# Kernel tuning notes

Hardware: AMD Instinct MI355X
Metric: run time of the kernel (lower is better)

Reference implementation:

```python
import jax, jax.numpy as jnp
import numpy as np

# Hard-coded dims from MambaLayer.__init__
D_IN = 20        # input feature dim (Dense infers it; chosen = modelInternalDim)
D_INNER = 20     # modelInternalDim
N_STATES = 10    # modelStates
DT_RANK = 5      # delta_t_rank
BATCH = 4
SEQ = 32768


def setup_inputs() -> dict:
    key = jax.random.key(0)
    ks = jax.random.split(key, 8)
    s = lambda k, shape: jax.random.normal(k, shape, dtype=jnp.float32) * 0.05
    A = jnp.tile(jnp.arange(1, N_STATES + 1, dtype=jnp.float32)[None, :], (D_INNER, 1))
    return {
        "x": jax.random.normal(ks[0], (BATCH, SEQ, D_IN), dtype=jnp.float32),
        "w_in": s(ks[1], (D_IN, 2 * D_INNER)),
        "b_in": jnp.zeros((2 * D_INNER,), jnp.float32),
        "conv_k": s(ks[2], (3, D_INNER, D_INNER)),   # (W, I, O)
        "conv_b": jnp.zeros((D_INNER,), jnp.float32),
        "w_x": s(ks[3], (D_INNER, DT_RANK + 2 * N_STATES)),
        "b_x": jnp.zeros((DT_RANK + 2 * N_STATES,), jnp.float32),
        "w_dt": s(ks[4], (DT_RANK, D_INNER)),
        "b_dt": jnp.zeros((D_INNER,), jnp.float32),
        "A_log": jnp.log(A),
        "D_param": jnp.ones((D_INNER,), jnp.float32),
    }


def _selective_scan(u, delta, A, B, C, D):
    # u, delta: (b,l,d); A: (d,n); B, C: (b,l,n); D: (d,)
    dA = jnp.einsum('bld,dn->bldn', delta, A)                  # (b,l,d,n)
    dB_u = jnp.einsum('bld,bld,bln->bldn', delta, u, B)        # (b,l,d,n)
    # tf.pad(dA[:,1:], [[0,0],[1,1],...])[:,1:] == concat(dA[:,1:], zeros) along l
    dA_shift = jnp.concatenate([dA[:, 1:], jnp.zeros_like(dA[:, :1])], axis=1)
    # reversed cumsum, exponentiate, reverse back
    dA_cumsum = jnp.exp(jnp.flip(jnp.cumsum(jnp.flip(dA_shift, axis=1), axis=1), axis=1))
    x = jnp.cumsum(dB_u * dA_cumsum, axis=1) / (dA_cumsum + 1e-12)
    y = jnp.einsum('bldn,bln->bld', x, C)
    return y + u * D


def reference(x, w_in, b_in, conv_k, conv_b, w_x, b_x, w_dt, b_dt, A_log, D_param):
    # in_projection + split (res half is unused, matching the original call())
    h = x @ w_in + b_in                                        # (b,l,2d)
    h, _res = jnp.split(h, 2, axis=-1)
    # causal Conv1D, kernel_size=3: left-pad by 2
    h = jax.lax.conv_general_dilated(
        h, conv_k, window_strides=(1,), padding=[(2, 0)],
        dimension_numbers=('NWC', 'WIO', 'NWC')) + conv_b
    h = jax.nn.silu(h)                                         # tf.nn.swish
    # ssm
    A = -jnp.exp(A_log)                                        # (d,n)
    xp = h @ w_x + b_x                                         # (b,l,r+2n)
    delta = xp[..., :DT_RANK]
    Bm = xp[..., DT_RANK:DT_RANK + N_STATES]
    Cm = xp[..., DT_RANK + N_STATES:]
    delta = jax.nn.softmax(delta @ w_dt + b_dt, axis=-1)       # (b,l,d)
    return _selective_scan(h, delta, A, Bm, Cm, D_param)
```

## Files before the change

kernel.cpp:

```cpp
#include <hip/hip_runtime.h>
#include <math.h>

#define B_   4
#define L_   32768
#define DI   20
#define NS   10
#define TBLK 128
#define NCB  256

#define OFF_AP   0u
#define OFF_RS   204800u
#define OFF_SC   409600u
#define OFF_TOT  430080u
#define OFF_H16  430192u
#define OFF_CMIN 4362352u
#define HD  0u
#define HU  2621440u
#define HB  5242880u
#define HC  6553600u

typedef _Float16 h16;
typedef _Float16 half8 __attribute__((ext_vector_type(8)));
typedef _Float16 half4 __attribute__((ext_vector_type(4)));
typedef float f32x4 __attribute__((ext_vector_type(4)));

template<int CTRL>
__device__ __forceinline__ float dppf(float idv, float src) {
    union U { float f; int i; };
    U o, s, r; o.f = idv; s.f = src;
    r.i = __builtin_amdgcn_update_dpp(o.i, s.i, CTRL, 0xf, 0xf, false);
    return r.f;
}
#define ROW_SHR1 0x111
#define ROW_SHR2 0x112
#define ROW_SHR4 0x114
#define ROW_SHR8 0x118

#define OPSCAN16(Ac, Bc) \
    { float aP = dppf<ROW_SHR1>(1.0f, Ac); float bP = dppf<ROW_SHR1>(0.0f, Bc); \
      Bc = fmaf(Ac, bP, Bc); Ac *= aP; \
      aP = dppf<ROW_SHR2>(1.0f, Ac); bP = dppf<ROW_SHR2>(0.0f, Bc); \
      Bc = fmaf(Ac, bP, Bc); Ac *= aP; \
      aP = dppf<ROW_SHR4>(1.0f, Ac); bP = dppf<ROW_SHR4>(0.0f, Bc); \
      Bc = fmaf(Ac, bP, Bc); Ac *= aP; \
      aP = dppf<ROW_SHR8>(1.0f, Ac); bP = dppf<ROW_SHR8>(0.0f, Bc); \
      Bc = fmaf(Ac, bP, Bc); Ac *= aP; }

#define SUMSCAN16(v) \
    { v += dppf<ROW_SHR1>(0.0f, v); v += dppf<ROW_SHR2>(0.0f, v); \
      v += dppf<ROW_SHR4>(0.0f, v); v += dppf<ROW_SHR8>(0.0f, v); }

#define XS_   0
#define MT_   2640
#define UL_   0
#define DS__  0
#define DUS_  2720
#define XP5_  4608
#define BS_   5448
#define WXo   6808
#define WDTo  7808
#define BDTo  7908
#define BXo   7928
#define POOLH 7956
#define WF_   7956
#define POOL2 (POOLH + 3200)

__global__ __launch_bounds__(320) void k1(
    const float* __restrict__ x,
    const float* __restrict__ w_in, const float* __restrict__ b_in,
    const float* __restrict__ conv_k, const float* __restrict__ conv_b,
    const float* __restrict__ w_x, const float* __restrict__ b_x,
    const float* __restrict__ w_dt, const float* __restrict__ b_dt,
    const float* __restrict__ A_log, const float* __restrict__ D_param,
    h16* __restrict__ dh, h16* __restrict__ uh,
    h16* __restrict__ Bh, h16* __restrict__ Ch,
    float* __restrict__ ap_ws, float* __restrict__ rs_ws, float* __restrict__ sc_ws,
    float* __restrict__ out)
{
    __shared__ __align__(16) h16 P[POOL2];
    __shared__ float beff_s[20];
    __shared__ float ALs[200];
    __shared__ float D_s[20];

    const int tid = threadIdx.x;
    const int c   = blockIdx.x;
    const int b   = blockIdx.y;
    const int l0  = c * TBLK;

    {
        float* Wf = (float*)&P[WF_];
        for (int i = tid; i < 400;  i += 320) Wf[i]       = w_in[(i/20)*40 + (i%20)];
        for (int i = tid; i < 1200; i += 320) Wf[400 + i] = conv_k[i];
        for (int i = tid; i < 200;  i += 320) ALs[i] = -__expf(A_log[i]);
        if (tid < 20) D_s[tid] = D_param[tid];
    }
    __syncthreads();

    {
        const float* Wf = (const float*)&P[WF_];
        for (int e = tid; e < 1200; e += 320) {
            int cc = e/20, o = e - cc*20;
            int w = cc/20, i = cc - w*20;
            float acc = 0.0f;
            #pragma unroll
            for (int op = 0; op < 20; op++)
                acc = fmaf(Wf[i*20 + op], Wf[400 + (w*20 + op)*20 + o], acc);
            P[MT_ + o*72 + cc] = (h16)acc;
        }
        for (int i = tid; i < 240; i += 320) {
            int o = i/12, cc = 60 + (i - (i/12)*12);
            P[MT_ + o*72 + cc] = (h16)0.0f;
        }
        for (int i = tid; i < 1000; i += 320) {
            int j = i/40, k = i - j*40;
            P[WXo + i] = (k < 20) ? (h16)w_x[k*25 + j] : (h16)0.0f;
        }
        for (int i = tid; i < 100; i += 320) P[WDTo + i] = (h16)w_dt[i];
        if (tid < 20) P[BDTo + tid] = (h16)b_dt[tid];
        if (tid < 25) P[BXo + tid] = (h16)b_x[tid];
        if (tid < 20) {
            float be = conv_b[tid];
            #pragma unroll
            for (int w = 0; w < 3; w++)
                #pragma unroll
                for (int op = 0; op < 20; op++)
                    be = fmaf(b_in[op], Wf[400 + (w*20 + op)*20 + tid], be);
            beff_s[tid] = be;
        }
        const float* xb = x + ((size_t)b*L_ + l0)*DI - 2*DI;
        for (int i = tid; i < 1320; i += 320) {
            float2 v;
            if (i >= 1300 || (c == 0 && i < 20)) v = make_float2(0.0f, 0.0f);
            else v = *(const float2*)(xb + 2*i);
            P[XS_ + 2*i]     = (h16)v.x;
            P[XS_ + 2*i + 1] = (h16)v.y;
        }
    }
    __syncthreads();

    const int wv  = tid >> 6;
    const int ln  = tid & 63;
    const int m16 = ln & 15;
    const int q   = ln >> 4;
    float uval[4][4];
    if (wv < 4) {
        #pragma unroll
        for (int jj = 0; jj < 4; jj++) {
            int job = wv*4 + jj, mt = job >> 1, nt = job & 1;
            int t_row = mt*16 + m16;
            int dcol  = nt*16 + m16;
            int dmin  = dcol < 20 ? dcol : 19;
            f32x4 acc = {0.0f, 0.0f, 0.0f, 0.0f};
            #pragma unroll
            for (int kh = 0; kh < 2; kh++) {
                half8 af, bf;
                int ab = XS_ + t_row*20 + kh*32 + (q<<3);
                *(half4*)&af         = *(const half4*)&P[ab];
                *(((half4*)&af) + 1) = *(const half4*)&P[ab + 4];
                int bb = MT_ + dmin*72 + kh*32 + (q<<3);
                *(half4*)&bf         = *(const half4*)&P[bb];
                *(((half4*)&bf) + 1) = *(const half4*)&P[bb + 4];
                acc = __builtin_amdgcn_mfma_f32_16x16x32_f16(af, bf, acc, 0, 0, 0);
            }
            float bfv = beff_s[dmin];
            #pragma unroll
            for (int r = 0; r < 4; r++) {
                float a = acc[r] + bfv;
                uval[jj][r] = a * __builtin_amdgcn_rcpf(1.0f + __expf(-a));
            }
        }
    }
    __syncthreads();

    if (wv < 4) {
        #pragma unroll
        for (int jj = 0; jj < 4; jj++) {
            int job = wv*4 + jj, mt = job >> 1, nt = job & 1;
            int dcol = nt*16 + m16;
            if (dcol < 20) {
                #pragma unroll
                for (int r = 0; r < 4; r++)
                    P[UL_ + (mt*16 + q*4 + r)*36 + dcol] = (h16)uval[jj][r];
            }
        }
    }
    __syncthreads();

    float xv[4][4];
    if (wv < 4) {
        #pragma unroll
        for (int jj = 0; jj < 4; jj++) {
            int job = wv*4 + jj, mt = job >> 1, nt = job & 1;
            int t_row = mt*16 + m16;
            int j     = nt*16 + m16;
            int jmin  = j < 25 ? j : 24;
            f32x4 acc = {0.0f, 0.0f, 0.0f, 0.0f};
            half8 af, bf;
            int ab = UL_ + t_row*36 + (q<<3);
            *(half4*)&af         = *(const half4*)&P[ab];
            *(((half4*)&af) + 1) = *(const half4*)&P[ab + 4];
            int bb = WXo + jmin*40 + (q<<3);
            *(half4*)&bf         = *(const half4*)&P[bb];
            *(((half4*)&bf) + 1) = *(const half4*)&P[bb + 4];
            acc = __builtin_amdgcn_mfma_f32_16x16x32_f16(af, bf, acc, 0, 0, 0);
            float bx = (j < 25) ? (float)P[BXo + j] : 0.0f;
            #pragma unroll
            for (int r = 0; r < 4; r++) xv[jj][r] = acc[r] + bx;
        }
        #pragma unroll
        for (int jj = 0; jj < 4; jj++) {
            int job = wv*4 + jj, mt = job >> 1, nt = job & 1;
            int j = nt*16 + m16;
            #pragma unroll
            for (int r = 0; r < 4; r++) {
                int t = mt*16 + q*4 + r;
                h16 hv = (h16)xv[jj][r];
                if (j < 5)       P[XP5_ + t*5 + j] = hv;
                else if (j < 15) P[BS_ + (j - 5)*136 + t] = hv;
                else if (j < 25) Ch[(size_t)(b*NS + (j - 15))*L_ + l0 + t] = hv;
            }
        }
    }
    __syncthreads();

    h16 urow[20];
    float dl[20];
    if (tid < 128) {
        const int t = tid;
        *(half4*)&urow[0]  = *(const half4*)&P[UL_ + t*36 + 0];
        *(half4*)&urow[4]  = *(const half4*)&P[UL_ + t*36 + 4];
        *(half4*)&urow[8]  = *(const half4*)&P[UL_ + t*36 + 8];
        *(half4*)&urow[12] = *(const half4*)&P[UL_ + t*36 + 12];
        *(half4*)&urow[16] = *(const half4*)&P[UL_ + t*36 + 16];
        #pragma unroll
        for (int d2 = 0; d2 < 20; d2++)
            uh[(size_t)(b*DI + d2)*L_ + l0 + t] = urow[d2];
        #pragma unroll
        for (int n = 0; n < NS; n++)
            Bh[(size_t)(b*NS + n)*L_ + l0 + t] = P[BS_ + n*136 + t];
        {
            float yo[20];
            #pragma unroll
            for (int d2 = 0; d2 < 20; d2++) yo[d2] = (float)urow[d2] * D_s[d2];
            float4* ob = (float4*)(out + ((size_t)b*L_ + l0 + t)*DI);
            #pragma unroll
            for (int k4 = 0; k4 < 5; k4++)
                ob[k4] = make_float4(yo[4*k4], yo[4*k4+1], yo[4*k4+2], yo[4*k4+3]);
        }
        float xq[5];
        #pragma unroll
        for (int r = 0; r < 5; r++) xq[r] = (float)P[XP5_ + t*5 + r];
        #pragma unroll
        for (int d2 = 0; d2 < 20; d2++) dl[d2] = (float)P[BDTo + d2];
        #pragma unroll
        for (int r = 0; r < 5; r++) {
            float dv = xq[r];
            #pragma unroll
            for (int d2 = 0; d2 < 20; d2++)
                dl[d2] = fmaf(dv, (float)P[WDTo + r*20 + d2], dl[d2]);
        }
        float mx = dl[0];
        #pragma unroll
        for (int d2 = 1; d2 < 20; d2++) mx = fmaxf(mx, dl[d2]);
        float sm = 0.0f;
        #pragma unroll
        for (int d2 = 0; d2 < 20; d2++) { dl[d2] = __expf(dl[d2] - mx); sm += dl[d2]; }
        float inv = __builtin_amdgcn_rcpf(sm);
        #pragma unroll
        for (int d2 = 0; d2 < 20; d2++) dl[d2] *= inv;
    }
    __syncthreads();

    if (tid < 128) {
        const int t = tid;
        #pragma unroll
        for (int d2 = 0; d2 < 20; d2++) {
            h16 dlh = (h16)dl[d2];
            P[DS__ + d2*136 + t] = dlh;
            P[DUS_ + d2*136 + t] = (h16)((float)dlh * (float)urow[d2]);
            dh[(size_t)(b*DI + d2)*L_ + l0 + t] = dlh;
        }
    }
    __syncthreads();

    const int d  = tid >> 4;
    const int s  = tid & 15;
    const int bd = b*DI + d;

    float d8[8], du8[8];
    { half8 hv = *(const half8*)&P[DS__ + d*136 + 8*s];
      #pragma unroll
      for (int j = 0; j < 8; j++) d8[j] = (float)hv[j]; }
    { half8 hv = *(const half8*)&P[DUS_ + d*136 + 8*s];
      #pragma unroll
      for (int j = 0; j < 8; j++) du8[j] = (float)hv[j]; }

    float loc8 = 0.0f;
    #pragma unroll
    for (int j = 0; j < 8; j++) loc8 += d8[j];
    float ssum = loc8;
    SUMSCAN16(ssum);
    if (s == 15) sc_ws[(size_t)bd*NCB + c] = ssum;

    float A_dn[NS];
    #pragma unroll
    for (int n = 0; n < NS; n++) A_dn[n] = ALs[d*NS + n];

    bool fastA = true;
    #pragma unroll
    for (int n = 1; n < NS; n++)
        fastA = fastA &&
            (fabsf(A_dn[n] - (float)(n+1)*A_dn[0]) <= 1e-3f*fabsf(A_dn[n]) + 1e-6f);

    float AcA[NS], BcA[NS];
    if (fastA) {
        float e1[8], ep[8];
        #pragma unroll
        for (int j = 0; j < 8; j++) { e1[j] = __expf(A_dn[0]*d8[j]); ep[j] = e1[j]; }
        #pragma unroll
        for (int n = 0; n < NS; n++) {
            half8 bv = *(const half8*)&P[BS_ + n*136 + 8*s];
            float Bc = 0.0f;
            #pragma unroll
            for (int j = 0; j < 8; j++)
                Bc = fmaf(ep[j], Bc, du8[j]*(float)bv[j]);
            BcA[n] = Bc;
            AcA[n] = __expf(A_dn[n]*loc8);
            if (n < NS-1) {
                #pragma unroll
                for (int j = 0; j < 8; j++) ep[j] *= e1[j];
            }
        }
    } else {
        #pragma unroll
        for (int n = 0; n < NS; n++) {
            half8 bv = *(const half8*)&P[BS_ + n*136 + 8*s];
            float Bc = 0.0f;
            #pragma unroll
            for (int j = 0; j < 8; j++) {
                float a = __expf(A_dn[n]*d8[j]);
                Bc = fmaf(a, Bc, du8[j]*(float)bv[j]);
            }
            BcA[n] = Bc;
            AcA[n] = __expf(A_dn[n]*loc8);
        }
    }
    #pragma unroll
    for (int n = 0; n < NS; n++) { OPSCAN16(AcA[n], BcA[n]); }
    if (s == 15) {
        const size_t o0 = ((size_t)bd*NS)*NCB + c;
        #pragma unroll
        for (int n = 0; n < NS; n++) {
            ap_ws[o0 + (size_t)n*NCB] = AcA[n];
            rs_ws[o0 + (size_t)n*NCB] = BcA[n];
        }
    }
}

__global__ __launch_bounds__(64) void kC2(
    const float* __restrict__ ap_ws, float* __restrict__ rs_ws,
    float* __restrict__ sc_ws, float* __restrict__ tot_ws,
    const float* __restrict__ A_log, float* __restrict__ cmin_ws)
{
    const int bd   = blockIdx.x;
    const int lane = threadIdx.x;
    const size_t sb = (size_t)bd*NCB + lane*4;

    float4 sv = *(const float4*)(sc_ws + sb);
    float l1 = sv.x, l2 = l1 + sv.y, l3 = l2 + sv.z, l4 = l3 + sv.w;
    float inc = l4;
    #pragma unroll
    for (int off = 1; off < 64; off <<= 1) {
        float t = __shfl_up(inc, off);
        if (lane >= off) inc += t;
    }
    float ex = __shfl_up(inc, 1);
    if (lane == 0) ex = 0.0f;
    *(float4*)(sc_ws + sb) = make_float4(ex, ex + l1, ex + l2, ex + l3);
    if (lane == 63) tot_ws[bd] = inc;

    {
        const float TotAll = __shfl(inc, 63);
        const int dd = bd % DI;
        float mnlog = A_log[dd*NS];
        #pragma unroll
        for (int n = 1; n < NS; n++) mnlog = fminf(mnlog, A_log[dd*NS + n]);
        const float Amax = -__expf(mnlog);
        int cand = 100000;
        if (fmaf(Amax, TotAll - (ex + l4), 40.0f) > 0.0f) cand = lane*4 + 3;
        if (fmaf(Amax, TotAll - (ex + l3), 40.0f) > 0.0f) cand = lane*4 + 2;
        if (fmaf(Amax, TotAll - (ex + l2), 40.0f) > 0.0f) cand = lane*4 + 1;
        if (fmaf(Amax, TotAll - (ex + l1), 40.0f) > 0.0f) cand = lane*4 + 0;
        #pragma unroll
        for (int off = 32; off > 0; off >>= 1)
            cand = min(cand, __shfl_xor(cand, off));
        if (lane == 0) cmin_ws[bd] = (float)cand;
    }

    #pragma unroll 2
    for (int n = 0; n < NS; n++) {
        const size_t base = ((size_t)bd*NS + n)*NCB + lane*4;
        float4 av = *(const float4*)(ap_ws + base);
        float4 rv = *(const float4*)(rs_ws + base);
        float Ac = av.x, Bc = rv.x;
        Bc = fmaf(av.y, Bc, rv.y); Ac *= av.y;
        Bc = fmaf(av.z, Bc, rv.z); Ac *= av.z;
        Bc = fmaf(av.w, Bc, rv.w); Ac *= av.w;
        #pragma unroll
        for (int off = 1; off < 64; off <<= 1) {
            float aP = __shfl_up(Ac, off);
            float bP = __shfl_up(Bc, off);
            if (lane >= off) { Bc = fmaf(Ac, bP, Bc); Ac *= aP; }
        }
        float pB = __shfl_up(Bc, 1);
        if (lane == 0) pB = 0.0f;
        float r  = pB;
        float o0 = r; r = fmaf(av.x, r, rv.x);
        float o1 = r; r = fmaf(av.y, r, rv.y);
        float o2 = r; r = fmaf(av.z, r, rv.z);
        float o3 = r;
        *(float4*)(rs_ws + base) = make_float4(o0, o1, o2, o3);
    }
}

__global__ __launch_bounds__(320) void kD(
    const h16* __restrict__ dh, const h16* __restrict__ uh,
    const h16* __restrict__ Bh, const h16* __restrict__ Ch,
    const float* __restrict__ A_log, const float* __restrict__ D_param,
    const float* __restrict__ rs_ws, const float* __restrict__ sc_ws,
    const float* __restrict__ tot_ws, const float* __restrict__ cmin_ws,
    float* __restrict__ out)
{
    __shared__ float ylT[20*132];
    __shared__ int anyact;
    const int tid = threadIdx.x;
    const int d   = tid >> 4;
    const int s   = tid & 15;
    const int c   = blockIdx.x;
    const int b   = blockIdx.y;
    const int bd  = b*DI + d;
    const size_t t0 = (size_t)c*TBLK + s*8;

    const bool active = (c >= (int)cmin_ws[bd]);

    if (tid == 0) anyact = 0;
    __syncthreads();
    if (active) anyact = 1;
    __syncthreads();
    if (anyact == 0) return;

    float u8[8];
    { half8 hv = *(const half8*)(uh + (size_t)bd*L_ + t0);
      #pragma unroll
      for (int j = 0; j < 8; j++) u8[j] = (float)hv[j]; }
    const float Dd = D_param[d];
    float yv[8];
    #pragma unroll
    for (int j = 0; j < 8; j++) yv[j] = u8[j]*Dd;

    if (active) {
        half8 dvv = *(const half8*)(dh + (size_t)bd*L_ + t0);
        half8 bvA[NS], cvA[NS];
        #pragma unroll
        for (int n = 0; n < NS; n++) {
            bvA[n] = *(const half8*)(Bh + (size_t)(b*NS + n)*L_ + t0);
            cvA[n] = *(const half8*)(Ch + (size_t)(b*NS + n)*L_ + t0);
        }
        float rin[NS];
        #pragma unroll
        for (int n = 0; n < NS; n++) rin[n] = rs_ws[((size_t)bd*NS + n)*NCB + c];
        const float Tot = tot_ws[bd];
        const float scc = sc_ws[(size_t)bd*NCB + c];
        float A_dn[NS];
        #pragma unroll
        for (int n = 0; n < NS; n++) A_dn[n] = -__expf(A_log[d*NS + n]);

        bool fastA = true;
        #pragma unroll
        for (int n = 1; n < NS; n++)
            fastA = fastA &&
                (fabsf(A_dn[n] - (float)(n+1)*A_dn[0]) <= 1e-3f*fabsf(A_dn[n]) + 1e-6f);

        float d8[8], du8[8];
        #pragma unroll
        for (int j = 0; j < 8; j++) { d8[j] = (float)dvv[j]; du8[j] = d8[j]*u8[j]; }

        float lp[8];
        { float run = 0.0f;
          #pragma unroll
          for (int j = 0; j < 8; j++) { run += d8[j]; lp[j] = run; } }
        float inc = lp[7];
        SUMSCAN16(inc);
        float ex = dppf<ROW_SHR1>(0.0f, inc);
        const float basep = scc + ex;

        float yacc[8];
        #pragma unroll
        for (int j = 0; j < 8; j++) yacc[j] = 0.0f;

        if (fastA) {
            float e1[8], ep[8];
            #pragma unroll
            for (int j = 0; j < 8; j++) { e1[j] = __expf(A_dn[0]*d8[j]); ep[j] = e1[j]; }
            #pragma unroll
            for (int n = 0; n < NS; n++) {
                float b8[8];
                #pragma unroll
                for (int j = 0; j < 8; j++) b8[j] = du8[j]*(float)bvA[n][j];
                float Bc = 0.0f;
                #pragma unroll
                for (int j = 0; j < 8; j++) Bc = fmaf(ep[j], Bc, b8[j]);
                float Ac = __expf(A_dn[n]*lp[7]);
                OPSCAN16(Ac, Bc);
                float pA = dppf<ROW_SHR1>(1.0f, Ac);
                float pB = dppf<ROW_SHR1>(0.0f, Bc);
                float r  = fmaf(pA, rin[n], pB);

                float G[8];
                G[7] = __expf(A_dn[n]*(Tot - (basep + lp[7])));
                #pragma unroll
                for (int j = 6; j >= 0; j--) G[j] = G[j+1]*ep[j+1];
                #pragma unroll
                for (int j = 0; j < 8; j++) {
                    r = fmaf(ep[j], r, b8[j]);
                    float damp = G[j] * __builtin_amdgcn_rcpf(G[j] + 1e-12f);
                    yacc[j] = fmaf((float)cvA[n][j]*damp, r, yacc[j]);
                }
                if (n < NS-1) {
                    #pragma unroll
                    for (int j = 0; j < 8; j++) ep[j] *= e1[j];
                }
            }
        } else {
            #pragma unroll 2
            for (int n = 0; n < NS; n++) {
                float a8[8], b8[8];
                #pragma unroll
                for (int j = 0; j < 8; j++) {
                    a8[j] = __expf(A_dn[n]*d8[j]);
                    b8[j] = du8[j]*(float)bvA[n][j];
                }
                float Bc = 0.0f;
                #pragma unroll
                for (int j = 0; j < 8; j++) Bc = fmaf(a8[j], Bc, b8[j]);
                float Ac = __expf(A_dn[n]*lp[7]);
                OPSCAN16(Ac, Bc);
                float pA = dppf<ROW_SHR1>(1.0f, Ac);
                float pB = dppf<ROW_SHR1>(0.0f, Bc);
                float r  = fmaf(pA, rin[n], pB);

                float G[8];
                G[7] = __expf(A_dn[n]*(Tot - (basep + lp[7])));
                #pragma unroll
                for (int j = 6; j >= 0; j--) G[j] = G[j+1]*a8[j+1];
                #pragma unroll
                for (int j = 0; j < 8; j++) {
                    r = fmaf(a8[j], r, b8[j]);
                    float damp = G[j] * __builtin_amdgcn_rcpf(G[j] + 1e-12f);
                    yacc[j] = fmaf((float)cvA[n][j]*damp, r, yacc[j]);
                }
            }
        }
        #pragma unroll
        for (int j = 0; j < 8; j++) yv[j] = fmaf(u8[j], Dd, yacc[j]);
    }

    *(float4*)&ylT[d*132 + 8*s]     = *(float4*)(yv);
    *(float4*)&ylT[d*132 + 8*s + 4] = *(float4*)(yv + 4);
    __syncthreads();

    float4* ob4 = (float4*)(out + ((size_t)b*L_ + (size_t)c*TBLK)*DI);
    for (int i = tid; i < TBLK*DI/4; i += 320) {
        int t = i / 5, qq = (i - t*5)*4;
        ob4[i] = make_float4(ylT[qq*132 + t], ylT[(qq+1)*132 + t],
                             ylT[(qq+2)*132 + t], ylT[(qq+3)*132 + t]);
    }
}

extern "C" void kernel_launch(void* const* d_in, const int* in_sizes, int n_in,
                              void* d_out, int out_size, void* d_ws, size_t ws_size,
                              hipStream_t stream) {
    const float* x      = (const float*)d_in[0];
    const float* w_in   = (const float*)d_in[1];
    const float* b_in   = (const float*)d_in[2];
    const float* conv_k = (const float*)d_in[3];
    const float* conv_b = (const float*)d_in[4];
    const float* w_x    = (const float*)d_in[5];
    const float* b_x    = (const float*)d_in[6];
    const float* w_dt   = (const float*)d_in[7];
    const float* b_dt   = (const float*)d_in[8];
    const float* A_log  = (const float*)d_in[9];
    const float* D_par  = (const float*)d_in[10];
    float* out = (float*)d_out;
    float* ws  = (float*)d_ws;

    float* ap_ws   = ws + OFF_AP;
    float* rs_ws   = ws + OFF_RS;
    float* sc_ws   = ws + OFF_SC;
    float* tot_ws  = ws + OFF_TOT;
    float* cmin_ws = ws + OFF_CMIN;
    h16*   hbase   = (h16*)(ws + OFF_H16);
    h16* dh  = hbase + HD;
    h16* uh  = hbase + HU;
    h16* Bh  = hbase + HB;
    h16* Ch  = hbase + HC;

    k1<<<dim3(NCB, B_), 320, 0, stream>>>(x, w_in, b_in, conv_k, conv_b,
                                          w_x, b_x, w_dt, b_dt, A_log, D_par,
                                          dh, uh, Bh, Ch,
                                          ap_ws, rs_ws, sc_ws, out);
    kC2<<<B_*DI, 64, 0, stream>>>(ap_ws, rs_ws, sc_ws, tot_ws, A_log, cmin_ws);
    kD<<<dim3(NCB, B_), 320, 0, stream>>>(dh, uh, Bh, Ch, A_log, D_par,
                                          rs_ws, sc_ws, tot_ws, cmin_ws, out);
}
```

Before: 123.6 us.

## Fuse carry scan and tail output pass into one per-channel kernel

Merges the chunk-carry scan kernel and the output kernel into a single kernel with one 64-thread block per (batch, channel). Scanned prefix sums and carries stay in shared memory instead of going back to the workspace. Each block then loops only over its own active tail chunks, four at a time, and writes outputs directly. This removes one launch and several workspace round trips, and drops the grid of mostly-idle output blocks. The cost is far less parallelism for the tail work, since only 80 small blocks run, and output stores are now strided per channel instead of coalesced through a shared-memory transpose.

```diff
diff --git a/kernel.cpp b/kernel.cpp
--- a/kernel.cpp
+++ b/kernel.cpp
@@ -11,9 +11,7 @@
 #define OFF_AP   0u
 #define OFF_RS   204800u
 #define OFF_SC   409600u
-#define OFF_TOT  430080u
 #define OFF_H16  430192u
-#define OFF_CMIN 4362352u
 #define HD  0u
 #define HU  2621440u
 #define HB  5242880u
@@ -357,15 +355,22 @@
     }
 }
 
-__global__ __launch_bounds__(64) void kC2(
-    const float* __restrict__ ap_ws, float* __restrict__ rs_ws,
-    float* __restrict__ sc_ws, float* __restrict__ tot_ws,
-    const float* __restrict__ A_log, float* __restrict__ cmin_ws)
+__global__ __launch_bounds__(64) void kC3(
+    const float* __restrict__ ap_ws, const float* __restrict__ rs_ws,
+    const float* __restrict__ sc_ws, const float* __restrict__ A_log,
+    const float* __restrict__ D_param,
+    const h16* __restrict__ dh, const h16* __restrict__ uh,
+    const h16* __restrict__ Bh, const h16* __restrict__ Ch,
+    float* __restrict__ out)
 {
+    __shared__ float sc_l[NCB];
+    __shared__ float rs_l[NS][NCB];
     const int bd   = blockIdx.x;
     const int lane = threadIdx.x;
+    const int b    = bd / DI;
+    const int d    = bd - b*DI;
+
     const size_t sb = (size_t)bd*NCB + lane*4;
-
     float4 sv = *(const float4*)(sc_ws + sb);
     float l1 = sv.x, l2 = l1 + sv.y, l3 = l2 + sv.z, l4 = l3 + sv.w;
     float inc = l4;
@@ -376,26 +381,21 @@
     }
     float ex = __shfl_up(inc, 1);
     if (lane == 0) ex = 0.0f;
-    *(float4*)(sc_ws + sb) = make_float4(ex, ex + l1, ex + l2, ex + l3);
-    if (lane == 63) tot_ws[bd] = inc;
-
-    {
-        const float TotAll = __shfl(inc, 63);
-        const int dd = bd % DI;
-        float mnlog = A_log[dd*NS];
-        #pragma unroll
-        for (int n = 1; n < NS; n++) mnlog = fminf(mnlog, A_log[dd*NS + n]);
-        const float Amax = -__expf(mnlog);
-        int cand = 100000;
-        if (fmaf(Amax, TotAll - (ex + l4), 40.0f) > 0.0f) cand = lane*4 + 3;
-        if (fmaf(Amax, TotAll - (ex + l3), 40.0f) > 0.0f) cand = lane*4 + 2;
-        if (fmaf(Amax, TotAll - (ex + l2), 40.0f) > 0.0f) cand = lane*4 + 1;
-        if (fmaf(Amax, TotAll - (ex + l1), 40.0f) > 0.0f) cand = lane*4 + 0;
-        #pragma unroll
-        for (int off = 32; off > 0; off >>= 1)
-            cand = min(cand, __shfl_xor(cand, off));
-        if (lane == 0) cmin_ws[bd] = (float)cand;
-    }
+    *(float4*)(&sc_l[lane*4]) = make_float4(ex, ex + l1, ex + l2, ex + l3);
+    const float Tot = __shfl(inc, 63);
+
+    float mnlog = A_log[d*NS];
+    #pragma unroll
+    for (int n = 1; n < NS; n++) mnlog = fminf(mnlog, A_log[d*NS + n]);
+    const float Amax = -__expf(mnlog);
+    int cand = NCB;
+    if (fmaf(Amax, Tot - (ex + l4), 40.0f) > 0.0f) cand = lane*4 + 3;
+    if (fmaf(Amax, Tot - (ex + l3), 40.0f) > 0.0f) cand = lane*4 + 2;
+    if (fmaf(Amax, Tot - (ex + l2), 40.0f) > 0.0f) cand = lane*4 + 1;
+    if (fmaf(Amax, Tot - (ex + l1), 40.0f) > 0.0f) cand = lane*4 + 0;
+    #pragma unroll
+    for (int off = 32; off > 0; off >>= 1)
+        cand = min(cand, __shfl_xor(cand, off));
 
     #pragma unroll 2
     for (int n = 0; n < NS; n++) {
@@ -418,162 +418,131 @@
         float o0 = r; r = fmaf(av.x, r, rv.x);
         float o1 = r; r = fmaf(av.y, r, rv.y);
         float o2 = r; r = fmaf(av.z, r, rv.z);
-        float o3 = r;
-        *(float4*)(rs_ws + base) = make_float4(o0, o1, o2, o3);
-    }
-}
-
-__global__ __launch_bounds__(320) void kD(
-    const h16* __restrict__ dh, const h16* __restrict__ uh,
-    const h16* __restrict__ Bh, const h16* __restrict__ Ch,
-    const float* __restrict__ A_log, const float* __restrict__ D_param,
-    const float* __restrict__ rs_ws, const float* __restrict__ sc_ws,
-    const float* __restrict__ tot_ws, const float* __restrict__ cmin_ws,
-    float* __restrict__ out)
-{
-    __shared__ float ylT[20*132];
-    __shared__ int anyact;
-    const int tid = threadIdx.x;
-    const int d   = tid >> 4;
-    const int s   = tid & 15;
-    const int c   = blockIdx.x;
-    const int b   = blockIdx.y;
-    const int bd  = b*DI + d;
-    const size_t t0 = (size_t)c*TBLK + s*8;
-
-    const bool active = (c >= (int)cmin_ws[bd]);
-
-    if (tid == 0) anyact = 0;
-    __syncthreads();
-    if (active) anyact = 1;
-    __syncthreads();
-    if (anyact == 0) return;
-
-    float u8[8];
-    { half8 hv = *(const half8*)(uh + (size_t)bd*L_ + t0);
-      #pragma unroll
-      for (int j = 0; j < 8; j++) u8[j] = (float)hv[j]; }
+        *(float4*)(&rs_l[n][lane*4]) = make_float4(o0, o1, o2, r);
+    }
+    __syncthreads();
+
+    if (cand >= NCB) return;
+    const int cmin = cand;
+
+    float A_dn[NS];
+    #pragma unroll
+    for (int n = 0; n < NS; n++) A_dn[n] = -__expf(A_log[d*NS + n]);
+    bool fastA = true;
+    #pragma unroll
+    for (int n = 1; n < NS; n++)
+        fastA = fastA &&
+            (fabsf(A_dn[n] - (float)(n+1)*A_dn[0]) <= 1e-3f*fabsf(A_dn[n]) + 1e-6f);
     const float Dd = D_param[d];
-    float yv[8];
-    #pragma unroll
-    for (int j = 0; j < 8; j++) yv[j] = u8[j]*Dd;
-
-    if (active) {
-        half8 dvv = *(const half8*)(dh + (size_t)bd*L_ + t0);
-        half8 bvA[NS], cvA[NS];
-        #pragma unroll
-        for (int n = 0; n < NS; n++) {
-            bvA[n] = *(const half8*)(Bh + (size_t)(b*NS + n)*L_ + t0);
-            cvA[n] = *(const half8*)(Ch + (size_t)(b*NS + n)*L_ + t0);
-        }
-        float rin[NS];
-        #pragma unroll
-        for (int n = 0; n < NS; n++) rin[n] = rs_ws[((size_t)bd*NS + n)*NCB + c];
-        const float Tot = tot_ws[bd];
-        const float scc = sc_ws[(size_t)bd*NCB + c];
-        float A_dn[NS];
-        #pragma unroll
-        for (int n = 0; n < NS; n++) A_dn[n] = -__expf(A_log[d*NS + n]);
-
-        bool fastA = true;
-        #pragma unroll
-        for (int n = 1; n < NS; n++)
-            fastA = fastA &&
-                (fabsf(A_dn[n] - (float)(n+1)*A_dn[0]) <= 1e-3f*fabsf(A_dn[n]) + 1e-6f);
-
-        float d8[8], du8[8];
-        #pragma unroll
-        for (int j = 0; j < 8; j++) { d8[j] = (float)dvv[j]; du8[j] = d8[j]*u8[j]; }
-
-        float lp[8];
-        { float run = 0.0f;
-          #pragma unroll
-          for (int j = 0; j < 8; j++) { run += d8[j]; lp[j] = run; } }
-        float inc = lp[7];
-        SUMSCAN16(inc);
-        float ex = dppf<ROW_SHR1>(0.0f, inc);
-        const float basep = scc + ex;
-
-        float yacc[8];
-        #pragma unroll
-        for (int j = 0; j < 8; j++) yacc[j] = 0.0f;
-
-        if (fastA) {
-            float e1[8], ep[8];
-            #pragma unroll
-            for (int j = 0; j < 8; j++) { e1[j] = __expf(A_dn[0]*d8[j]); ep[j] = e1[j]; }
+    const int g = lane >> 4;
+    const int s = lane & 15;
+
+    for (int cb = cmin; cb < NCB; cb += 4) {
+        const int c = cb + g;
+        if (c < NCB) {
+            const size_t t0 = (size_t)c*TBLK + s*8;
+            half8 uvv = *(const half8*)(uh + (size_t)bd*L_ + t0);
+            half8 dvv = *(const half8*)(dh + (size_t)bd*L_ + t0);
+            half8 bvA[NS], cvA[NS];
             #pragma unroll
             for (int n = 0; n < NS; n++) {
-                float b8[8];
+                bvA[n] = *(const half8*)(Bh + (size_t)(b*NS + n)*L_ + t0);
+                cvA[n] = *(const half8*)(Ch + (size_t)(b*NS + n)*L_ + t0);
+            }
+            float rin[NS];
+            #pragma unroll
+            for (int n = 0; n < NS; n++) rin[n] = rs_l[n][c];
+            const float scc = sc_l[c];
+
+            float u8[8], d8[8], du8[8];
+            #pragma unroll
+            for (int j = 0; j < 8; j++) {
+                u8[j] = (float)uvv[j];
+                d8[j] = (float)dvv[j];
+                du8[j] = d8[j]*u8[j];
+            }
+            float lp[8];
+            { float run = 0.0f;
+              #pragma unroll
+              for (int j = 0; j < 8; j++) { run += d8[j]; lp[j] = run; } }
+            float inc2 = lp[7];
+            SUMSCAN16(inc2);
+            float ex2 = dppf<ROW_SHR1>(0.0f, inc2);
+            const float basep = scc + ex2;
+
+            float yacc[8];
+            #pragma unroll
+            for (int j = 0; j < 8; j++) yacc[j] = 0.0f;
+
+            if (fastA) {
+                float e1[8], ep[8];
                 #pragma unroll
-                for (int j = 0; j < 8; j++) b8[j] = du8[j]*(float)bvA[n][j];
-                float Bc = 0.0f;
+                for (int j = 0; j < 8; j++) { e1[j] = __expf(A_dn[0]*d8[j]); ep[j] = e1[j]; }
                 #pragma unroll
-                for (int j = 0; j < 8; j++) Bc = fmaf(ep[j], Bc, b8[j]);
-                float Ac = __expf(A_dn[n]*lp[7]);
-                OPSCAN16(Ac, Bc);
-                float pA = dppf<ROW_SHR1>(1.0f, Ac);
-                float pB = dppf<ROW_SHR1>(0.0f, Bc);
-                float r  = fmaf(pA, rin[n], pB);
-
-                float G[8];
-                G[7] = __expf(A_dn[n]*(Tot - (basep + lp[7])));
-                #pragma unroll
-                for (int j = 6; j >= 0; j--) G[j] = G[j+1]*ep[j+1];
-                #pragma unroll
-                for (int j = 0; j < 8; j++) {
-                    r = fmaf(ep[j], r, b8[j]);
-                    float damp = G[j] * __builtin_amdgcn_rcpf(G[j] + 1e-12f);
-                    yacc[j] = fmaf((float)cvA[n][j]*damp, r, yacc[j]);
+                for (int n = 0; n < NS; n++) {
+                    float b8[8];
+                    #pragma unroll
+                    for (int j = 0; j < 8; j++) b8[j] = du8[j]*(float)bvA[n][j];
+                    float Bc = 0.0f;
+                    #pragma unroll
+                    for (int j = 0; j < 8; j++) Bc = fmaf(ep[j], Bc, b8[j]);
+                    float Ac = __expf(A_dn[n]*lp[7]);
+                    OPSCAN16(Ac, Bc);
+                    float pA = dppf<ROW_SHR1>(1.0f, Ac);
+                    float pB = dppf<ROW_SHR1>(0.0f, Bc);
+                    float r  = fmaf(pA, rin[n], pB);
+
+                    float G[8];
+                    G[7] = __expf(A_dn[n]*(Tot - (basep + lp[7])));
+                    #pragma unroll
+                    for (int j = 6; j >= 0; j--) G[j] = G[j+1]*ep[j+1];
+                    #pragma unroll
+                    for (int j = 0; j < 8; j++) {
+                        r = fmaf(ep[j], r, b8[j]);
+                        float damp = G[j] * __builtin_amdgcn_rcpf(G[j] + 1e-12f);
+                        yacc[j] = fmaf((float)cvA[n][j]*damp, r, yacc[j]);
+                    }
+                    if (n < NS-1) {
+                        #pragma unroll
+                        for (int j = 0; j < 8; j++) ep[j] *= e1[j];
+                    }
                 }
-                if (n < NS-1) {
-                    #pragma unroll
-                    for (int j = 0; j < 8; j++) ep[j] *= e1[j];
+            } else {
+                #pragma unroll 2
+                for (int n = 0; n < NS; n++) {
+                    float a8[8], b8[8];
+                    #pragma unroll
+                    for (int j = 0; j < 8; j++) {
+                        a8[j] = __expf(A_dn[n]*d8[j]);
+                        b8[j] = du8[j]*(float)bvA[n][j];
+                    }
+                    float Bc = 0.0f;
+                    #pragma unroll
+                    for (int j = 0; j < 8; j++) Bc = fmaf(a8[j], Bc, b8[j]);
+                    float Ac = __expf(A_dn[n]*lp[7]);
+                    OPSCAN16(Ac, Bc);
+                    float pA = dppf<ROW_SHR1>(1.0f, Ac);
+                    float pB = dppf<ROW_SHR1>(0.0f, Bc);
+                    float r  = fmaf(pA, rin[n], pB);
+
+                    float G[8];
+                    G[7] = __expf(A_dn[n]*(Tot - (basep + lp[7])));
+                    #pragma unroll
+                    for (int j = 6; j >= 0; j--) G[j] = G[j+1]*a8[j+1];
+                    #pragma unroll
+                    for (int j = 0; j < 8; j++) {
+                        r = fmaf(a8[j], r, b8[j]);
+                        float damp = G[j] * __builtin_amdgcn_rcpf(G[j] + 1e-12f);
+                        yacc[j] = fmaf((float)cvA[n][j]*damp, r, yacc[j]);
+                    }
                 }
             }
-        } else {
-            #pragma unroll 2
-            for (int n = 0; n < NS; n++) {
-                float a8[8], b8[8];
-                #pragma unroll
-                for (int j = 0; j < 8; j++) {
-                    a8[j] = __expf(A_dn[n]*d8[j]);
-                    b8[j] = du8[j]*(float)bvA[n][j];
-                }
-                float Bc = 0.0f;
-                #pragma unroll
-                for (int j = 0; j < 8; j++) Bc = fmaf(a8[j], Bc, b8[j]);
-                float Ac = __expf(A_dn[n]*lp[7]);
-                OPSCAN16(Ac, Bc);
-                float pA = dppf<ROW_SHR1>(1.0f, Ac);
-                float pB = dppf<ROW_SHR1>(0.0f, Bc);
-                float r  = fmaf(pA, rin[n], pB);
-
-                float G[8];
-                G[7] = __expf(A_dn[n]*(Tot - (basep + lp[7])));
-                #pragma unroll
-                for (int j = 6; j >= 0; j--) G[j] = G[j+1]*a8[j+1];
-                #pragma unroll
-                for (int j = 0; j < 8; j++) {
-                    r = fmaf(a8[j], r, b8[j]);
-                    float damp = G[j] * __builtin_amdgcn_rcpf(G[j] + 1e-12f);
-                    yacc[j] = fmaf((float)cvA[n][j]*damp, r, yacc[j]);
-                }
-            }
-        }
-        #pragma unroll
-        for (int j = 0; j < 8; j++) yv[j] = fmaf(u8[j], Dd, yacc[j]);
-    }
-
-    *(float4*)&ylT[d*132 + 8*s]     = *(float4*)(yv);
-    *(float4*)&ylT[d*132 + 8*s + 4] = *(float4*)(yv + 4);
-    __syncthreads();
-
-    float4* ob4 = (float4*)(out + ((size_t)b*L_ + (size_t)c*TBLK)*DI);
-    for (int i = tid; i < TBLK*DI/4; i += 320) {
-        int t = i / 5, qq = (i - t*5)*4;
-        ob4[i] = make_float4(ylT[qq*132 + t], ylT[(qq+1)*132 + t],
-                             ylT[(qq+2)*132 + t], ylT[(qq+3)*132 + t]);
+
+            float* ob = out + ((size_t)b*L_ + t0)*DI + d;
+            #pragma unroll
+            for (int j = 0; j < 8; j++)
+                ob[j*DI] = fmaf(u8[j], Dd, yacc[j]);
+        }
     }
 }
 
@@ -594,12 +563,10 @@
     float* out = (float*)d_out;
     float* ws  = (float*)d_ws;
 
-    float* ap_ws   = ws + OFF_AP;
-    float* rs_ws   = ws + OFF_RS;
-    float* sc_ws   = ws + OFF_SC;
-    float* tot_ws  = ws + OFF_TOT;
-    float* cmin_ws = ws + OFF_CMIN;
-    h16*   hbase   = (h16*)(ws + OFF_H16);
+    float* ap_ws = ws + OFF_AP;
+    float* rs_ws = ws + OFF_RS;
+    float* sc_ws = ws + OFF_SC;
+    h16*   hbase = (h16*)(ws + OFF_H16);
     h16* dh  = hbase + HD;
     h16* uh  = hbase + HU;
     h16* Bh  = hbase + HB;
@@ -609,7 +576,6 @@
                                           w_x, b_x, w_dt, b_dt, A_log, D_par,
                                           dh, uh, Bh, Ch,
                                           ap_ws, rs_ws, sc_ws, out);
-    kC2<<<B_*DI, 64, 0, stream>>>(ap_ws, rs_ws, sc_ws, tot_ws, A_log, cmin_ws);
-    kD<<<dim3(NCB, B_), 320, 0, stream>>>(dh, uh, Bh, Ch, A_log, D_par,
-                                          rs_ws, sc_ws, tot_ws, cmin_ws, out);
+    kC3<<<B_*DI, 64, 0, stream>>>(ap_ws, rs_ws, sc_ws, A_log, D_par,
+                                  dh, uh, Bh, Ch, out);
 }
```

Result: faster. 108.6 us (median of 2 runs) (-12.2%).
